# Kernel tuning notes

Measured on AMD Instinct MI355X. Metric: run time of the kernel, lower is better.

The kernel has to match this reference:

```python
import jax, jax.numpy as jnp
from jax import lax
import numpy as np

NPOINT1, RADIUS1, NSAMPLE1 = 2048, 0.4, 32
NPOINT2, RADIUS2, NSAMPLE2 = 512, 0.8, 64


def _fps(xyz, npoint):
    # Farthest point sampling (deterministic start at index 0). xyz: (N,3)
    N = xyz.shape[0]
    def step(carry, _):
        dists, farthest = carry
        centroid = xyz[farthest]                      # (3,)
        d = jnp.sum((xyz - centroid) ** 2, axis=-1)   # (N,)
        dists = jnp.minimum(dists, d)
        return (dists, jnp.argmax(dists).astype(jnp.int32)), farthest
    init = (jnp.full((N,), 1e10, xyz.dtype), jnp.asarray(0, jnp.int32))
    _, idx = lax.scan(step, init, None, length=npoint)
    return idx                                        # (npoint,) int32


def _ball_query(radius, nsample, xyz, new_xyz):
    # For each centroid pick up to nsample neighbor indices within radius,
    # padding with the first found index (centroid itself is always in range).
    N = xyz.shape[0]
    sqr = jnp.sum((new_xyz[:, None, :] - xyz[None, :, :]) ** 2, axis=-1)  # (S,N)
    cand = jnp.where(sqr <= radius * radius,
                     jnp.arange(N, dtype=jnp.int32)[None, :], N)
    neg, _ = lax.top_k(-cand, nsample)   # smallest nsample valid indices
    idx = -neg
    first = idx[:, :1]
    return jnp.where(idx == N, first, idx)            # (S, nsample)


def _mlp(h, ws, bs, contract):
    # Per-point shared MLP (1x1 conv + folded-BN bias + ReLU)
    for w, b in zip(ws, bs):
        h = jax.nn.relu(jnp.einsum(contract, h, w) + b)
    return h


def _sa(xyz, feats, npoint, radius, nsample, ws, bs):
    new_xyz = xyz[_fps(xyz, npoint)]                  # (S,3)
    gidx = _ball_query(radius, nsample, xyz, new_xyz) # (S,K)
    grouped_xyz = xyz[gidx] - new_xyz[:, None, :]     # (S,K,3) centered
    h = jnp.concatenate([grouped_xyz, feats[gidx]], axis=-1)  # (S,K,3+C)
    h = _mlp(h, ws, bs, 'skc,oc->sko')
    return new_xyz, jnp.max(h, axis=1)                # (S,C_out)


def _sa_all(xyz, feats, ws, bs):
    # group_all stage: single group over all remaining points
    h = jnp.concatenate([xyz, feats], axis=-1)        # (S,3+C)
    h = _mlp(h, ws, bs, 'sc,oc->so')
    return jnp.max(h, axis=0)                         # (C_out,)


def _forward(points, proposal, w1, b1, w2, b2, w3, b3):
    x, y, w = proposal[0], proposal[1], proposal[3]
    zero = jnp.zeros_like(x)
    xyz = points - jnp.stack([x, y, zero])            # centre-normalized coords
    offs = [(x + w / 2, y), (x - w / 2, y), (x, y + w / 2), (x, y - w / 2)]
    feats = jnp.concatenate(
        [points - jnp.stack([ox, oy, zero]) for ox, oy in offs], axis=-1)  # (N,12)
    xyz1, f1 = _sa(xyz, feats, NPOINT1, RADIUS1, NSAMPLE1, w1, b1)
    xyz2, f2 = _sa(xyz1, f1, NPOINT2, RADIUS2, NSAMPLE2, w2, b2)
    return _sa_all(xyz2, f2, w3, b3)                  # (1024,)


def setup_inputs() -> dict:
    key = jax.random.key(0)
    k = jax.random.split(key, 40)
    N = 32768
    inp = {}
    inp['points'] = jax.random.normal(k[0], (N, 3), jnp.float32)
    inp['proposal'] = jax.random.uniform(k[1], (6,), jnp.float32, 0.1, 1.0)
    dims = {'sa1': [(64, 15), (64, 64), (128, 64)],
            'sa2': [(128, 131), (128, 128), (256, 128)],
            'sa3': [(256, 259), (512, 256), (1024, 512)]}
    ki = 2
    for name, layer_dims in dims.items():
        for i, (o, c) in enumerate(layer_dims):
            inp[f'{name}_w{i}'] = jax.random.normal(k[ki], (o, c), jnp.float32) / np.float32(np.sqrt(c)); ki += 1
            inp[f'{name}_b{i}'] = jax.random.normal(k[ki], (o,), jnp.float32) * 0.02; ki += 1
    return inp


def reference(points, proposal,
              sa1_w0, sa1_w1, sa1_w2, sa1_b0, sa1_b1, sa1_b2,
              sa2_w0, sa2_w1, sa2_w2, sa2_b0, sa2_b1, sa2_b2,
              sa3_w0, sa3_w1, sa3_w2, sa3_b0, sa3_b1, sa3_b2):
    return _forward(points, proposal,
                    [sa1_w0, sa1_w1, sa1_w2], [sa1_b0, sa1_b1, sa1_b2],
                    [sa2_w0, sa2_w1, sa2_w2], [sa2_b0, sa2_b1, sa2_b2],
                    [sa3_w0, sa3_w1, sa3_w2], [sa3_b0, sa3_b1, sa3_b2])
```

## Files before the change

kernel.cpp:

```cpp
#include <hip/hip_runtime.h>
#include <cstdint>
#include <cstddef>

typedef unsigned long long ull;

#define N_PTS  32768
#define NP1    2048
#define NSAMP1 32
#define NP2    512
#define NSAMP2 64

__global__ __launch_bounds__(256) void k_prep(const float* __restrict__ pts,
                                              const float* __restrict__ prop,
                                              float* __restrict__ xx,
                                              float* __restrict__ xy,
                                              float* __restrict__ xz) {
  int t = blockIdx.x * 256 + threadIdx.x;
  if (t >= N_PTS) return;
  float x = prop[0], y = prop[1];
  xx[t] = __fsub_rn(pts[3 * t + 0], x);
  xy[t] = __fsub_rn(pts[3 * t + 1], y);
  xz[t] = pts[3 * t + 2];
}

#define F1T 512
#define F1P 64
#define F1R 33
#define F1L (F1P - F1R)

__global__ __launch_bounds__(F1T, 2) void k_fps1(const float* __restrict__ xx,
                                                 const float* __restrict__ xy,
                                                 const float* __restrict__ xz,
                                                 float* __restrict__ ox,
                                                 float* __restrict__ oy,
                                                 float* __restrict__ oz) {
  __shared__ float pzl[F1L * F1T];
  __shared__ float wmax[F1T / 64];
  __shared__ int S[2];
  int tid = threadIdx.x;
  float px[F1P], py[F1P], pzr[F1R], d[F1P];
#pragma unroll
  for (int s = 0; s < F1P; ++s) {
    int i = s * F1T + tid;
    px[s] = xx[i];
    py[s] = xy[i];
    float z = xz[i];
    if (s < F1R) pzr[s] = z;
    else pzl[(s - F1R) * F1T + tid] = z;
    d[s] = 1e10f;
  }
  if (tid == 0) { S[0] = 0; S[1] = 0x7fffffff; }
  __syncthreads();
  for (int it = 0; it < NP1; ++it) {
    int f = __builtin_amdgcn_readfirstlane(S[it & 1]);
    float cx = xx[f], cy = xy[f], cz = xz[f];
    if (tid == 0) { ox[it] = cx; oy[it] = cy; oz[it] = cz; }
    float bestv = -1.0f;
#pragma unroll
    for (int s = 0; s < F1P; ++s) {
      float z = (s < F1R) ? pzr[s] : pzl[(s - F1R) * F1T + tid];
      float dx = __fsub_rn(px[s], cx);
      float dy = __fsub_rn(py[s], cy);
      float dz = __fsub_rn(z, cz);
      float d2 = __fadd_rn(__fadd_rn(__fmul_rn(dx, dx), __fmul_rn(dy, dy)), __fmul_rn(dz, dz));
      float dn = fminf(d[s], d2);
      d[s] = dn;
      bestv = fmaxf(bestv, dn);
    }
    float wv = bestv;
#pragma unroll
    for (int m = 1; m < 64; m <<= 1) wv = fmaxf(wv, __shfl_xor(wv, m, 64));
    if ((tid & 63) == 0) wmax[tid >> 6] = wv;
    __syncthreads();
    float gb = wmax[0];
#pragma unroll
    for (int k = 1; k < F1T / 64; ++k) gb = fmaxf(gb, wmax[k]);
    if (bestv == gb) {
      int cand = 0x7fffffff;
#pragma unroll
      for (int s = F1P - 1; s >= 0; --s) cand = (d[s] == gb) ? (s * F1T + tid) : cand;
      atomicMin(&S[(it + 1) & 1], cand);
    }
    if (tid == 0) S[it & 1] = 0x7fffffff;
    __syncthreads();
  }
}

#define F2T 512
#define F2P 4
__global__ __launch_bounds__(F2T, 2) void k_fps2(const float* __restrict__ x1x,
                                                 const float* __restrict__ x1y,
                                                 const float* __restrict__ x1z,
                                                 float* __restrict__ ox,
                                                 float* __restrict__ oy,
                                                 float* __restrict__ oz) {
  __shared__ float sx[NP1], sy[NP1], sz[NP1];
  __shared__ float wmax[F2T / 64];
  __shared__ int S[2];
  int tid = threadIdx.x;
  float px[F2P], py[F2P], pz[F2P], d[F2P];
#pragma unroll
  for (int s = 0; s < F2P; ++s) {
    int i = s * F2T + tid;
    px[s] = x1x[i]; py[s] = x1y[i]; pz[s] = x1z[i];
    sx[i] = px[s];  sy[i] = py[s];  sz[i] = pz[s];
    d[s] = 1e10f;
  }
  if (tid == 0) { S[0] = 0; S[1] = 0x7fffffff; }
  __syncthreads();
  for (int it = 0; it < NP2; ++it) {
    int f = __builtin_amdgcn_readfirstlane(S[it & 1]);
    float cx = sx[f], cy = sy[f], cz = sz[f];
    if (tid == 0) { ox[it] = cx; oy[it] = cy; oz[it] = cz; }
    float bestv = -1.0f;
#pragma unroll
    for (int s = 0; s < F2P; ++s) {
      float dx = __fsub_rn(px[s], cx);
      float dy = __fsub_rn(py[s], cy);
      float dz = __fsub_rn(pz[s], cz);
      float d2 = __fadd_rn(__fadd_rn(__fmul_rn(dx, dx), __fmul_rn(dy, dy)), __fmul_rn(dz, dz));
      float dn = fminf(d[s], d2);
      d[s] = dn;
      bestv = fmaxf(bestv, dn);
    }
    float wv = bestv;
#pragma unroll
    for (int m = 1; m < 64; m <<= 1) wv = fmaxf(wv, __shfl_xor(wv, m, 64));
    if ((tid & 63) == 0) wmax[tid >> 6] = wv;
    __syncthreads();
    float gb = wmax[0];
#pragma unroll
    for (int k = 1; k < F2T / 64; ++k) gb = fmaxf(gb, wmax[k]);
    if (bestv == gb) {
      int cand = 0x7fffffff;
#pragma unroll
      for (int s = F2P - 1; s >= 0; --s) cand = (d[s] == gb) ? (s * F2T + tid) : cand;
      atomicMin(&S[(it + 1) & 1], cand);
    }
    if (tid == 0) S[it & 1] = 0x7fffffff;
    __syncthreads();
  }
}

__global__ void k_ballq(const float* __restrict__ px, const float* __restrict__ py,
                        const float* __restrict__ pz, int n,
                        const float* __restrict__ qx, const float* __restrict__ qy,
                        const float* __restrict__ qz, int S,
                        float r2, int ns, int* __restrict__ out) {
  int w = (blockIdx.x * (int)blockDim.x + threadIdx.x) >> 6;
  int lane = threadIdx.x & 63;
  if (w >= S) return;
  float cx = qx[w], cy = qy[w], cz = qz[w];
  int found = 0, first = 0;
  bool havefirst = false;
  for (int base = 0; base < n && found < ns; base += 64) {
    int i = base + lane;
    float dx = __fsub_rn(px[i], cx);
    float dy = __fsub_rn(py[i], cy);
    float dz = __fsub_rn(pz[i], cz);
    float d2 = __fadd_rn(__fadd_rn(__fmul_rn(dx, dx), __fmul_rn(dy, dy)), __fmul_rn(dz, dz));
    bool isin = d2 <= r2;
    ull m = __ballot(isin);
    if (!havefirst && m != 0ull) { first = base + __builtin_ctzll(m); havefirst = true; }
    if (isin) {
      int r = (int)__popcll(m & ((1ull << lane) - 1ull));
      int slot = found + r;
      if (slot < ns) out[w * ns + slot] = i;
    }
    found += (int)__popcll(m);
  }
  for (int s2 = found + lane; s2 < ns; s2 += 64) out[w * ns + s2] = first;
}

__global__ __launch_bounds__(256) void k_gather1(const float* __restrict__ pts,
                                                 const float* __restrict__ prop,
                                                 const float* __restrict__ xx,
                                                 const float* __restrict__ xy,
                                                 const float* __restrict__ xz,
                                                 const float* __restrict__ x1x,
                                                 const float* __restrict__ x1y,
                                                 const float* __restrict__ x1z,
                                                 const int* __restrict__ gidx,
                                                 float* __restrict__ X, int rbase) {
  int rl = blockIdx.x * 256 + threadIdx.x;
  if (rl >= 8192) return;
  int r = rbase + rl;
  int s = r >> 5;
  int g = gidx[r];
  float x = prop[0], y = prop[1], wz = prop[3];
  float w2 = wz * 0.5f;
  float oxp = __fadd_rn(x, w2), oxm = __fsub_rn(x, w2);
  float oyp = __fadd_rn(y, w2), oym = __fsub_rn(y, w2);
  float gx = xx[g], gy = xy[g], gz = xz[g];
  float pxv = pts[3 * g + 0], pyv = pts[3 * g + 1];
  float* o = X + (size_t)rl * 15;
  o[0] = __fsub_rn(gx, x1x[s]);
  o[1] = __fsub_rn(gy, x1y[s]);
  o[2] = __fsub_rn(gz, x1z[s]);
  o[3] = __fsub_rn(pxv, oxp);  o[4]  = gy;                    o[5]  = gz;
  o[6] = __fsub_rn(pxv, oxm);  o[7]  = gy;                    o[8]  = gz;
  o[9] = gx;                   o[10] = __fsub_rn(pyv, oyp);   o[11] = gz;
  o[12] = gx;                  o[13] = __fsub_rn(pyv, oym);   o[14] = gz;
}

__global__ __launch_bounds__(256) void k_gather2(const float* __restrict__ x1x,
                                                 const float* __restrict__ x1y,
                                                 const float* __restrict__ x1z,
                                                 const float* __restrict__ x2x,
                                                 const float* __restrict__ x2y,
                                                 const float* __restrict__ x2z,
                                                 const int* __restrict__ gidx,
                                                 const float* __restrict__ f1,
                                                 float* __restrict__ X, int rbase) {
  int e = blockIdx.x * 256 + threadIdx.x;
  if (e >= 8192 * 131) return;
  int rl = e / 131, c = e % 131;
  int r = rbase + rl;
  int s = r >> 6;
  int g = gidx[r];
  float v;
  if (c == 0)      v = __fsub_rn(x1x[g], x2x[s]);
  else if (c == 1) v = __fsub_rn(x1y[g], x2y[s]);
  else if (c == 2) v = __fsub_rn(x1z[g], x2z[s]);
  else             v = f1[(size_t)g * 128 + (c - 3)];
  X[e] = v;
}

__global__ __launch_bounds__(256) void k_gather3(const float* __restrict__ x2x,
                                                 const float* __restrict__ x2y,
                                                 const float* __restrict__ x2z,
                                                 const float* __restrict__ f2,
                                                 float* __restrict__ X) {
  int e = blockIdx.x * 256 + threadIdx.x;
  if (e >= 512 * 259) return;
  int rl = e / 259, c = e % 259;
  float v;
  if (c == 0)      v = x2x[rl];
  else if (c == 1) v = x2y[rl];
  else if (c == 2) v = x2z[rl];
  else             v = f2[(size_t)rl * 256 + (c - 3)];
  X[e] = v;
}

__global__ __launch_bounds__(256) void k_gemm(const float* __restrict__ A,
                                              const float* __restrict__ W,
                                              const float* __restrict__ bias,
                                              float* __restrict__ C,
                                              int M, int N, int K) {
  __shared__ __align__(16) float As[16][68];
  __shared__ __align__(16) float Bs[16][68];
  int tid = threadIdx.x;
  int bn = blockIdx.x * 64, bm = blockIdx.y * 64;
  int tx = tid & 15, ty = tid >> 4;
  float acc[4][4] = {{0.f, 0.f, 0.f, 0.f}, {0.f, 0.f, 0.f, 0.f},
                     {0.f, 0.f, 0.f, 0.f}, {0.f, 0.f, 0.f, 0.f}};
  for (int k0 = 0; k0 < K; k0 += 16) {
#pragma unroll
    for (int e = 0; e < 4; ++e) {
      int flat = tid + e * 256;
      int rr = flat >> 4, cc = flat & 15;
      As[cc][rr] = (k0 + cc < K) ? A[(size_t)(bm + rr) * K + (k0 + cc)] : 0.0f;
      Bs[cc][rr] = (k0 + cc < K) ? W[(size_t)(bn + rr) * K + (k0 + cc)] : 0.0f;
    }
    __syncthreads();
#pragma unroll
    for (int kk = 0; kk < 16; ++kk) {
      const float4 a = *(const float4*)&As[kk][ty * 4];
      const float4 b = *(const float4*)&Bs[kk][tx * 4];
      float av[4] = {a.x, a.y, a.z, a.w};
      float bb[4] = {b.x, b.y, b.z, b.w};
#pragma unroll
      for (int i = 0; i < 4; ++i)
#pragma unroll
        for (int j = 0; j < 4; ++j)
          acc[i][j] = fmaf(av[i], bb[j], acc[i][j]);
    }
    __syncthreads();
  }
#pragma unroll
  for (int i = 0; i < 4; ++i) {
    int m = bm + ty * 4 + i;
    float4 o;
    o.x = fmaxf(acc[i][0] + bias[bn + tx * 4 + 0], 0.0f);
    o.y = fmaxf(acc[i][1] + bias[bn + tx * 4 + 1], 0.0f);
    o.z = fmaxf(acc[i][2] + bias[bn + tx * 4 + 2], 0.0f);
    o.w = fmaxf(acc[i][3] + bias[bn + tx * 4 + 3], 0.0f);
    *(float4*)&C[(size_t)m * N + bn + tx * 4] = o;
  }
}

__global__ __launch_bounds__(256) void k_maxpool(const float* __restrict__ H,
                                                 float* __restrict__ F,
                                                 int S, int Ks, int Nch, int sbase) {
  int t = blockIdx.x * 256 + threadIdx.x;
  if (t >= S * Nch) return;
  int sl = t / Nch, n = t % Nch;
  const float* p = H + (size_t)sl * Ks * Nch + n;
  float m = p[0];
  for (int k = 1; k < Ks; ++k) m = fmaxf(m, p[(size_t)k * Nch]);
  F[(size_t)(sbase + sl) * Nch + n] = m;
}

extern "C" void kernel_launch(void* const* d_in, const int* in_sizes, int n_in,
                              void* d_out, int out_size, void* d_ws, size_t ws_size,
                              hipStream_t stream) {
  (void)n_in; (void)out_size; (void)ws_size;
  const float* pts = (const float*)d_in[0];
  const float* prop = (const float*)d_in[1];

  bool dict_order = (in_sizes[3] == 64);
  const float *w[3][3], *b[3][3];
  for (int g = 0; g < 3; ++g)
    for (int l = 0; l < 3; ++l) {
      int base = 2 + g * 6;
      int wi = dict_order ? (base + l * 2) : (base + l);
      int bi = dict_order ? (base + l * 2 + 1) : (base + 3 + l);
      w[g][l] = (const float*)d_in[wi];
      b[g][l] = (const float*)d_in[bi];
    }

  float* ws = (float*)d_ws;
  float* xx = ws;
  float* xy = xx + N_PTS;
  float* xz = xy + N_PTS;
  float* x1x = xz + N_PTS;
  float* x1y = x1x + NP1;
  float* x1z = x1y + NP1;
  float* x2x = x1z + NP1;
  float* x2y = x2x + NP2;
  float* x2z = x2y + NP2;
  int* gidx1 = (int*)(x2z + NP2);
  int* gidx2 = gidx1 + NP1 * NSAMP1;
  float* f1 = (float*)(gidx2 + NP2 * NSAMP2);
  float* f2 = f1 + NP1 * 128;
  float* Xp = f2 + NP2 * 256;
  float* Ha = Xp + 8192 * 131;
  float* Hb = Ha + 8192 * 128;
  float* Hc = Hb + 8192 * 128;

  const float R2A = (float)(0.4 * 0.4);
  const float R2B = (float)(0.8 * 0.8);

  k_prep<<<128, 256, 0, stream>>>(pts, prop, xx, xy, xz);
  k_fps1<<<1, F1T, 0, stream>>>(xx, xy, xz, x1x, x1y, x1z);
  k_fps2<<<1, F2T, 0, stream>>>(x1x, x1y, x1z, x2x, x2y, x2z);
  k_ballq<<<512, 256, 0, stream>>>(xx, xy, xz, N_PTS, x1x, x1y, x1z, NP1, R2A, NSAMP1, gidx1);
  k_ballq<<<128, 256, 0, stream>>>(x1x, x1y, x1z, NP1, x2x, x2y, x2z, NP2, R2B, NSAMP2, gidx2);

  for (int ch = 0; ch < 8; ++ch) {
    int rbase = ch * 8192;
    k_gather1<<<32, 256, 0, stream>>>(pts, prop, xx, xy, xz, x1x, x1y, x1z, gidx1, Xp, rbase);
    k_gemm<<<dim3(1, 128), 256, 0, stream>>>(Xp, w[0][0], b[0][0], Ha, 8192, 64, 15);
    k_gemm<<<dim3(1, 128), 256, 0, stream>>>(Ha, w[0][1], b[0][1], Hb, 8192, 64, 64);
    k_gemm<<<dim3(2, 128), 256, 0, stream>>>(Hb, w[0][2], b[0][2], Hc, 8192, 128, 64);
    k_maxpool<<<128, 256, 0, stream>>>(Hc, f1, 256, 32, 128, ch * 256);
  }

  for (int ch = 0; ch < 4; ++ch) {
    int rbase = ch * 8192;
    k_gather2<<<(8192 * 131 + 255) / 256, 256, 0, stream>>>(x1x, x1y, x1z, x2x, x2y, x2z,
                                                            gidx2, f1, Xp, rbase);
    k_gemm<<<dim3(2, 128), 256, 0, stream>>>(Xp, w[1][0], b[1][0], Ha, 8192, 128, 131);
    k_gemm<<<dim3(2, 128), 256, 0, stream>>>(Ha, w[1][1], b[1][1], Hb, 8192, 128, 128);
    k_gemm<<<dim3(4, 128), 256, 0, stream>>>(Hb, w[1][2], b[1][2], Hc, 8192, 256, 128);
    k_maxpool<<<128, 256, 0, stream>>>(Hc, f2, 128, 64, 256, ch * 128);
  }

  k_gather3<<<(512 * 259 + 255) / 256, 256, 0, stream>>>(x2x, x2y, x2z, f2, Xp);
  k_gemm<<<dim3(4, 8), 256, 0, stream>>>(Xp, w[2][0], b[2][0], Ha, 512, 256, 259);
  k_gemm<<<dim3(8, 8), 256, 0, stream>>>(Ha, w[2][1], b[2][1], Hb, 512, 512, 256);
  k_gemm<<<dim3(16, 8), 256, 0, stream>>>(Hb, w[2][2], b[2][2], Hc, 512, 1024, 512);
  k_maxpool<<<4, 256, 0, stream>>>(Hc, (float*)d_out, 1, 512, 1024, 0);
}
```

Before: 6.241 ms.

## Morton-sort points and prune far chunks in first farthest-point sampling

Adds a preprocessing pipeline that bins points into a Morton-ordered grid, scatters them into spatially sorted arrays and computes a bounding sphere per 64-point chunk. The first FPS pass then uses a 1024-thread block that, each iteration, skips chunks whose bounding sphere cannot lower any stored min-distance, and keeps per-chunk max keys in shared memory. The goal is to cut the O(N·npoint) distance updates of the serial FPS loop. Min-distances now live in global memory, and several extra small kernels are launched. Tie-breaking now follows sorted-array index rather than original index, and the scatter order is nondeterministic.

```diff
diff --git a/kernel.cpp b/kernel.cpp
--- a/kernel.cpp
+++ b/kernel.cpp
@@ -9,6 +9,7 @@
 #define NSAMP1 32
 #define NP2    512
 #define NSAMP2 64
+#define NCH    512
 
 __global__ __launch_bounds__(256) void k_prep(const float* __restrict__ pts,
                                               const float* __restrict__ prop,
@@ -23,66 +24,168 @@
   xz[t] = pts[3 * t + 2];
 }
 
-#define F1T 512
-#define F1P 64
-#define F1R 33
-#define F1L (F1P - F1R)
-
-__global__ __launch_bounds__(F1T, 2) void k_fps1(const float* __restrict__ xx,
+__device__ inline unsigned part3(unsigned v) {
+  v &= 31u;
+  v = (v | (v << 8)) & 0x0100Fu;
+  v = (v | (v << 4)) & 0x010C3u;
+  v = (v | (v << 2)) & 0x09249u;
+  return v;
+}
+
+__global__ __launch_bounds__(256) void k_morton(const float* __restrict__ xx,
+                                                const float* __restrict__ xy,
+                                                const float* __restrict__ xz,
+                                                int* __restrict__ mcode,
+                                                int* __restrict__ hist,
+                                                float* __restrict__ dmin) {
+  int i = blockIdx.x * 256 + threadIdx.x;
+  if (i >= N_PTS) return;
+  int bx = min(31, max(0, (int)floorf((xx[i] + 4.0f) * 4.0f)));
+  int by = min(31, max(0, (int)floorf((xy[i] + 4.0f) * 4.0f)));
+  int bz = min(31, max(0, (int)floorf((xz[i] + 4.0f) * 4.0f)));
+  int m = (int)(part3((unsigned)bx) | (part3((unsigned)by) << 1) | (part3((unsigned)bz) << 2));
+  mcode[i] = m;
+  atomicAdd(&hist[m], 1);
+  dmin[i] = 1e10f;
+}
+
+__global__ __launch_bounds__(1024) void k_scan(const int* __restrict__ hist,
+                                               int* __restrict__ off) {
+  __shared__ int ps[1024];
+  int t = threadIdx.x;
+  int base = t * 32;
+  int loc[32];
+  int s = 0;
+#pragma unroll
+  for (int i = 0; i < 32; ++i) { loc[i] = s; s += hist[base + i]; }
+  ps[t] = s;
+  __syncthreads();
+  for (int ofs = 1; ofs < 1024; ofs <<= 1) {
+    int v = (t >= ofs) ? ps[t - ofs] : 0;
+    __syncthreads();
+    ps[t] += v;
+    __syncthreads();
+  }
+  int ex = (t > 0) ? ps[t - 1] : 0;
+#pragma unroll
+  for (int i = 0; i < 32; ++i) off[base + i] = ex + loc[i];
+}
+
+__global__ __launch_bounds__(256) void k_scatter(const float* __restrict__ xx,
                                                  const float* __restrict__ xy,
                                                  const float* __restrict__ xz,
-                                                 float* __restrict__ ox,
-                                                 float* __restrict__ oy,
-                                                 float* __restrict__ oz) {
-  __shared__ float pzl[F1L * F1T];
-  __shared__ float wmax[F1T / 64];
-  __shared__ int S[2];
-  int tid = threadIdx.x;
-  float px[F1P], py[F1P], pzr[F1R], d[F1P];
-#pragma unroll
-  for (int s = 0; s < F1P; ++s) {
-    int i = s * F1T + tid;
-    px[s] = xx[i];
-    py[s] = xy[i];
-    float z = xz[i];
-    if (s < F1R) pzr[s] = z;
-    else pzl[(s - F1R) * F1T + tid] = z;
-    d[s] = 1e10f;
-  }
-  if (tid == 0) { S[0] = 0; S[1] = 0x7fffffff; }
+                                                 const int* __restrict__ mcode,
+                                                 int* __restrict__ off,
+                                                 float* __restrict__ sx,
+                                                 float* __restrict__ sy,
+                                                 float* __restrict__ sz,
+                                                 int* __restrict__ p0pos) {
+  int i = blockIdx.x * 256 + threadIdx.x;
+  if (i >= N_PTS) return;
+  int pos = atomicAdd(&off[mcode[i]], 1);
+  sx[pos] = xx[i];
+  sy[pos] = xy[i];
+  sz[pos] = xz[i];
+  if (i == 0) p0pos[0] = pos;
+}
+
+__global__ __launch_bounds__(64) void k_chunkb(const float* __restrict__ sx,
+                                               const float* __restrict__ sy,
+                                               const float* __restrict__ sz,
+                                               float4* __restrict__ cb) {
+  int ch = blockIdx.x, lane = threadIdx.x;
+  int i = ch * 64 + lane;
+  float x = sx[i], y = sy[i], z = sz[i];
+  float mnx = x, mxx = x, mny = y, mxy = y, mnz = z, mxz = z;
+#pragma unroll
+  for (int m = 1; m < 64; m <<= 1) {
+    mnx = fminf(mnx, __shfl_xor(mnx, m, 64)); mxx = fmaxf(mxx, __shfl_xor(mxx, m, 64));
+    mny = fminf(mny, __shfl_xor(mny, m, 64)); mxy = fmaxf(mxy, __shfl_xor(mxy, m, 64));
+    mnz = fminf(mnz, __shfl_xor(mnz, m, 64)); mxz = fmaxf(mxz, __shfl_xor(mxz, m, 64));
+  }
+  float cx = 0.5f * (mnx + mxx), cy = 0.5f * (mny + mxy), cz = 0.5f * (mnz + mxz);
+  float dx = x - cx, dy = y - cy, dz = z - cz;
+  float r2 = dx * dx + dy * dy + dz * dz;
+#pragma unroll
+  for (int m = 1; m < 64; m <<= 1) r2 = fmaxf(r2, __shfl_xor(r2, m, 64));
+  if (lane == 0) {
+    float r = sqrtf(r2) * 1.00002f + 1e-6f;
+    cb[ch] = make_float4(cx, cy, cz, r);
+  }
+}
+
+__global__ __launch_bounds__(1024, 1) void k_fps1p(const float* __restrict__ sx,
+                                                   const float* __restrict__ sy,
+                                                   const float* __restrict__ sz,
+                                                   const float4* __restrict__ cb,
+                                                   float* __restrict__ d,
+                                                   const int* __restrict__ p0pos,
+                                                   float* __restrict__ ox,
+                                                   float* __restrict__ oy,
+                                                   float* __restrict__ oz) {
+  __shared__ ull ckey[NCH];
+  __shared__ ull wpart[16];
+  __shared__ ull smask[8];
+  __shared__ int fsh;
+  int tid = threadIdx.x, lane = tid & 63, wv = tid >> 6;
+  if (tid < NCH) ckey[tid] = ((ull)__float_as_uint(1e10f) << 32) | 0xFFFFFFFFull;
+  if (tid == 0) fsh = p0pos[0];
   __syncthreads();
+  int f = fsh;
+  float cx = sx[f], cy = sy[f], cz = sz[f];
   for (int it = 0; it < NP1; ++it) {
-    int f = __builtin_amdgcn_readfirstlane(S[it & 1]);
-    float cx = xx[f], cy = xy[f], cz = xz[f];
     if (tid == 0) { ox[it] = cx; oy[it] = cy; oz[it] = cz; }
-    float bestv = -1.0f;
-#pragma unroll
-    for (int s = 0; s < F1P; ++s) {
-      float z = (s < F1R) ? pzr[s] : pzl[(s - F1R) * F1T + tid];
-      float dx = __fsub_rn(px[s], cx);
-      float dy = __fsub_rn(py[s], cy);
-      float dz = __fsub_rn(z, cz);
-      float d2 = __fadd_rn(__fadd_rn(__fmul_rn(dx, dx), __fmul_rn(dy, dy)), __fmul_rn(dz, dz));
-      float dn = fminf(d[s], d2);
-      d[s] = dn;
-      bestv = fmaxf(bestv, dn);
-    }
-    float wv = bestv;
-#pragma unroll
-    for (int m = 1; m < 64; m <<= 1) wv = fmaxf(wv, __shfl_xor(wv, m, 64));
-    if ((tid & 63) == 0) wmax[tid >> 6] = wv;
-    __syncthreads();
-    float gb = wmax[0];
-#pragma unroll
-    for (int k = 1; k < F1T / 64; ++k) gb = fmaxf(gb, wmax[k]);
-    if (bestv == gb) {
-      int cand = 0x7fffffff;
-#pragma unroll
-      for (int s = F1P - 1; s >= 0; --s) cand = (d[s] == gb) ? (s * F1T + tid) : cand;
-      atomicMin(&S[(it + 1) & 1], cand);
-    }
-    if (tid == 0) S[it & 1] = 0x7fffffff;
-    __syncthreads();
+    if (tid < NCH) {
+      float4 bsp = cb[tid];
+      float chmax = __uint_as_float((unsigned)(ckey[tid] >> 32));
+      float dx = cx - bsp.x, dy = cy - bsp.y, dz = cz - bsp.z;
+      float s = sqrtf(dx * dx + dy * dy + dz * dz);
+      float md = s * 0.99999f - bsp.w;
+      bool proc = !(md > 0.0f && md * md * 0.99999f > chmax * 1.00001f);
+      ull mb = __ballot(proc);
+      if (lane == 0) smask[wv] = mb;
+    }
+    __syncthreads();
+    for (int ch = wv; ch < NCH; ch += 16) {
+      if (!((smask[ch >> 6] >> (ch & 63)) & 1ull)) continue;
+      int idx = ch * 64 + lane;
+      float px = sx[idx], py = sy[idx], pz = sz[idx];
+      float dd = d[idx];
+      float ddx = __fsub_rn(px, cx);
+      float ddy = __fsub_rn(py, cy);
+      float ddz = __fsub_rn(pz, cz);
+      float d2 = __fadd_rn(__fadd_rn(__fmul_rn(ddx, ddx), __fmul_rn(ddy, ddy)),
+                           __fmul_rn(ddz, ddz));
+      float dn = fminf(dd, d2);
+      d[idx] = dn;
+      float wm = dn;
+#pragma unroll
+      for (int m = 1; m < 64; m <<= 1) wm = fmaxf(wm, __shfl_xor(wm, m, 64));
+      ull mk = __ballot(dn == wm);
+      int wl = __builtin_ctzll(mk);
+      if (lane == wl) ckey[ch] = ((ull)__float_as_uint(wm) << 32) | (unsigned)(~idx);
+    }
+    __syncthreads();
+    ull k = (tid < NCH) ? ckey[tid] : 0ull;
+#pragma unroll
+    for (int m = 1; m < 64; m <<= 1) {
+      ull o = __shfl_xor(k, m, 64);
+      k = (o > k) ? o : k;
+    }
+    if (lane == 0) wpart[wv] = k;
+    __syncthreads();
+    if (tid < 64) {
+      ull k2 = (lane < 16) ? wpart[lane] : 0ull;
+#pragma unroll
+      for (int m = 1; m < 16; m <<= 1) {
+        ull o = __shfl_xor(k2, m, 64);
+        k2 = (o > k2) ? o : k2;
+      }
+      if (lane == 0) fsh = (int)(~(unsigned)k2);
+    }
+    __syncthreads();
+    f = fsh;
+    cx = sx[f]; cy = sy[f]; cz = sz[f];
   }
 }
 
@@ -338,11 +441,25 @@
   float* Hb = Ha + 8192 * 128;
   float* Hc = Hb + 8192 * 128;
 
+  int*   mcode = (int*)Xp;
+  int*   hist  = mcode + N_PTS;
+  float* sxx   = (float*)(hist + N_PTS);
+  float* sxy   = sxx + N_PTS;
+  float* sxz   = sxy + N_PTS;
+  float* dmin  = sxz + N_PTS;
+  float4* cbv  = (float4*)(dmin + N_PTS);
+  int*   p0pos = (int*)(cbv + NCH);
+
   const float R2A = (float)(0.4 * 0.4);
   const float R2B = (float)(0.8 * 0.8);
 
   k_prep<<<128, 256, 0, stream>>>(pts, prop, xx, xy, xz);
-  k_fps1<<<1, F1T, 0, stream>>>(xx, xy, xz, x1x, x1y, x1z);
+  hipMemsetAsync(hist, 0, N_PTS * sizeof(int), stream);
+  k_morton<<<128, 256, 0, stream>>>(xx, xy, xz, mcode, hist, dmin);
+  k_scan<<<1, 1024, 0, stream>>>(hist, hist);
+  k_scatter<<<128, 256, 0, stream>>>(xx, xy, xz, mcode, hist, sxx, sxy, sxz, p0pos);
+  k_chunkb<<<NCH, 64, 0, stream>>>(sxx, sxy, sxz, cbv);
+  k_fps1p<<<1, 1024, 0, stream>>>(sxx, sxy, sxz, cbv, dmin, p0pos, x1x, x1y, x1z);
   k_fps2<<<1, F2T, 0, stream>>>(x1x, x1y, x1z, x2x, x2y, x2z);
   k_ballq<<<512, 256, 0, stream>>>(xx, xy, xz, N_PTS, x1x, x1y, x1z, NP1, R2A, NSAMP1, gidx1);
   k_ballq<<<128, 256, 0, stream>>>(x1x, x1y, x1z, NP1, x2x, x2y, x2z, NP2, R2B, NSAMP2, gidx2);
```

New measurement: 14.26 ms. 2.28x slower.

## Widen FPS1 to 1024 threads, keep z in LDS, broadcast centroid via shared

Applied to the files above, without the earlier changes.

The single-block farthest-point sampling kernel now uses 1024 threads with 32 points each instead of 512 threads with 64. All z coordinates move into 128KB of dynamic LDS. The winning thread writes the next centroid's coordinates into shared memory, so the per-iteration dependent global load of xx/xy/xz[f] goes away. This shortens the serial per-iteration chain but adds an extra __syncthreads per iteration and needs a large dynamic LDS allocation.

```diff
diff --git a/kernel.cpp b/kernel.cpp
--- a/kernel.cpp
+++ b/kernel.cpp
@@ -23,42 +23,41 @@
   xz[t] = pts[3 * t + 2];
 }
 
-#define F1T 512
-#define F1P 64
-#define F1R 33
-#define F1L (F1P - F1R)
-
-__global__ __launch_bounds__(F1T, 2) void k_fps1(const float* __restrict__ xx,
+#define F1T 1024
+#define F1P 32
+
+__global__ __launch_bounds__(F1T, 4) void k_fps1(const float* __restrict__ xx,
                                                  const float* __restrict__ xy,
                                                  const float* __restrict__ xz,
                                                  float* __restrict__ ox,
                                                  float* __restrict__ oy,
                                                  float* __restrict__ oz) {
-  __shared__ float pzl[F1L * F1T];
+  extern __shared__ float zs[];
   __shared__ float wmax[F1T / 64];
+  __shared__ float cc[2][3];
   __shared__ int S[2];
-  int tid = threadIdx.x;
-  float px[F1P], py[F1P], pzr[F1R], d[F1P];
+  int tid = threadIdx.x, lane = tid & 63, wv = tid >> 6;
+  float px[F1P], py[F1P], d[F1P];
 #pragma unroll
   for (int s = 0; s < F1P; ++s) {
     int i = s * F1T + tid;
     px[s] = xx[i];
     py[s] = xy[i];
-    float z = xz[i];
-    if (s < F1R) pzr[s] = z;
-    else pzl[(s - F1R) * F1T + tid] = z;
+    zs[i] = xz[i];
     d[s] = 1e10f;
   }
-  if (tid == 0) { S[0] = 0; S[1] = 0x7fffffff; }
+  if (tid == 0) {
+    S[0] = 0x7fffffff; S[1] = 0x7fffffff;
+    cc[0][0] = xx[0]; cc[0][1] = xy[0]; cc[0][2] = xz[0];
+  }
   __syncthreads();
   for (int it = 0; it < NP1; ++it) {
-    int f = __builtin_amdgcn_readfirstlane(S[it & 1]);
-    float cx = xx[f], cy = xy[f], cz = xz[f];
+    float cx = cc[it & 1][0], cy = cc[it & 1][1], cz = cc[it & 1][2];
     if (tid == 0) { ox[it] = cx; oy[it] = cy; oz[it] = cz; }
     float bestv = -1.0f;
 #pragma unroll
     for (int s = 0; s < F1P; ++s) {
-      float z = (s < F1R) ? pzr[s] : pzl[(s - F1R) * F1T + tid];
+      float z = zs[s * F1T + tid];
       float dx = __fsub_rn(px[s], cx);
       float dy = __fsub_rn(py[s], cy);
       float dz = __fsub_rn(z, cz);
@@ -67,19 +66,31 @@
       d[s] = dn;
       bestv = fmaxf(bestv, dn);
     }
-    float wv = bestv;
-#pragma unroll
-    for (int m = 1; m < 64; m <<= 1) wv = fmaxf(wv, __shfl_xor(wv, m, 64));
-    if ((tid & 63) == 0) wmax[tid >> 6] = wv;
+    float wm = bestv;
+#pragma unroll
+    for (int m = 1; m < 64; m <<= 1) wm = fmaxf(wm, __shfl_xor(wm, m, 64));
+    if (lane == 0) wmax[wv] = wm;
     __syncthreads();
     float gb = wmax[0];
 #pragma unroll
     for (int k = 1; k < F1T / 64; ++k) gb = fmaxf(gb, wmax[k]);
+    int n = (it + 1) & 1;
+    int cand = 0x7fffffff;
+    float ccx = 0.f, ccy = 0.f, ccz = 0.f;
     if (bestv == gb) {
-      int cand = 0x7fffffff;
-#pragma unroll
-      for (int s = F1P - 1; s >= 0; --s) cand = (d[s] == gb) ? (s * F1T + tid) : cand;
-      atomicMin(&S[(it + 1) & 1], cand);
+#pragma unroll
+      for (int s = 0; s < F1P; ++s) {
+        bool m = (d[s] == gb) && (cand == 0x7fffffff);
+        cand = m ? (s * F1T + tid) : cand;
+        ccx = m ? px[s] : ccx;
+        ccy = m ? py[s] : ccy;
+        ccz = m ? zs[s * F1T + tid] : ccz;
+      }
+      atomicMin(&S[n], cand);
+    }
+    __syncthreads();
+    if (cand != 0x7fffffff && cand == S[n]) {
+      cc[n][0] = ccx; cc[n][1] = ccy; cc[n][2] = ccz;
     }
     if (tid == 0) S[it & 1] = 0x7fffffff;
     __syncthreads();
@@ -340,9 +351,13 @@
 
   const float R2A = (float)(0.4 * 0.4);
   const float R2B = (float)(0.8 * 0.8);
+  const int F1LDS = N_PTS * (int)sizeof(float);
+
+  hipFuncSetAttribute((const void*)k_fps1,
+                      hipFuncAttributeMaxDynamicSharedMemorySize, F1LDS);
 
   k_prep<<<128, 256, 0, stream>>>(pts, prop, xx, xy, xz);
-  k_fps1<<<1, F1T, 0, stream>>>(xx, xy, xz, x1x, x1y, x1z);
+  k_fps1<<<1, F1T, F1LDS, stream>>>(xx, xy, xz, x1x, x1y, x1z);
   k_fps2<<<1, F2T, 0, stream>>>(x1x, x1y, x1z, x2x, x2y, x2z);
   k_ballq<<<512, 256, 0, stream>>>(xx, xy, xz, N_PTS, x1x, x1y, x1z, NP1, R2A, NSAMP1, gidx1);
   k_ballq<<<128, 256, 0, stream>>>(x1x, x1y, x1z, NP1, x2x, x2y, x2z, NP2, R2B, NSAMP2, gidx2);
```

Result: slower. 19.67 ms (+215.3%).
